# Performance work log

Hardware: AMD Instinct MI355X
Metric: run time of the kernel (lower is better)

## Reference

```python
import jax, jax.numpy as jnp
import numpy as np

ALPHA = 0.2  # LeakyReLU negative slope


def setup_inputs() -> dict:
    key = jax.random.key(0)
    ks = jax.random.split(key, 8)
    B, S, T, V, F = 8, 25, 64, 256, 256
    N = S * T
    h = jax.random.normal(ks[0], (B, S, T, V), dtype=jnp.float32)
    adj = jax.random.randint(ks[1], (N, N), 0, 2, dtype=jnp.int32)
    # xavier-ish scaling for stability
    W = jax.random.normal(ks[2], (F, V), dtype=jnp.float32) * (1.414 / np.sqrt(V))
    bW = jax.random.normal(ks[3], (F,), dtype=jnp.float32) * 0.01
    ai = jax.random.normal(ks[4], (1, F), dtype=jnp.float32) * (1.414 / np.sqrt(F))
    bi = jax.random.normal(ks[5], (1,), dtype=jnp.float32) * 0.01
    aj = jax.random.normal(ks[6], (1, F), dtype=jnp.float32) * (1.414 / np.sqrt(F))
    bj = jax.random.normal(ks[7], (1,), dtype=jnp.float32) * 0.01
    return {"h": h, "adj": adj, "W": W, "bW": bW, "ai": ai, "bi": bi, "aj": aj, "bj": bj}


def reference(h, adj, W, bW, ai, bi, aj, bj):
    B, S, T, V = h.shape
    N = S * T
    x = h.reshape(B, N, V)                    # [B, N, V]
    Wh = jnp.einsum('bnv,fv->bnf', x, W) + bW  # [B, N, F]
    Wh1 = jnp.einsum('bnf,of->bno', Wh, ai) + bi  # [B, N, 1]
    Wh2 = jnp.einsum('bnf,of->bno', Wh, aj) + bj  # [B, N, 1]
    e = Wh1 + jnp.swapaxes(Wh2, 1, 2)          # [B, N, N] additive scores
    e = jnp.where(e > 0, e, ALPHA * e)         # LeakyReLU
    att = jnp.where(adj[None, :, :] > 0, e, jnp.float32(-1e9))
    att = jax.nn.softmax(att, axis=2)          # masked softmax over neighbors
    h_hat = jnp.einsum('bij,bjf->bif', att, Wh)  # [B, N, F]
    return jax.nn.elu(h_hat)                   # concat=True path
```

## Files before the change

### kernel.cpp

```cpp
#include <hip/hip_runtime.h>
#include <hip/hip_bf16.h>

typedef __attribute__((ext_vector_type(8))) short bf16x8;
typedef __attribute__((ext_vector_type(4))) float f32x4;

#define LRELU_ALPHA 0.2f

static __device__ __forceinline__ unsigned short f2bf(float x) {
    unsigned u = __float_as_uint(x);
    u += 0x7fffu + ((u >> 16) & 1u);
    return (unsigned short)(u >> 16);
}
static __device__ __forceinline__ unsigned f2ord(float x) {
    unsigned b = __float_as_uint(x);
    return (b & 0x80000000u) ? ~b : (b | 0x80000000u);
}
static __device__ __forceinline__ float ord2f(unsigned m) {
    unsigned b = (m & 0x80000000u) ? (m ^ 0x80000000u) : ~m;
    return __uint_as_float(b);
}

__global__ __launch_bounds__(256) void k_convert(
    const float* __restrict__ x, const float* __restrict__ W,
    unsigned short* __restrict__ xb, unsigned short* __restrict__ Wb)
{
    const int bid = blockIdx.x;
    const float* src;
    unsigned short* dst;
    size_t base;
    if (bid < 1600) { src = x; dst = xb; base = (size_t)bid * 2048; }
    else            { src = W; dst = Wb; base = (size_t)(bid - 1600) * 2048; }
    const size_t idx = base + (size_t)threadIdx.x * 8;
    float4 v0 = *(const float4*)&src[idx];
    float4 v1 = *(const float4*)&src[idx + 4];
    ushort4 o0 = { f2bf(v0.x), f2bf(v0.y), f2bf(v0.z), f2bf(v0.w) };
    ushort4 o1 = { f2bf(v1.x), f2bf(v1.y), f2bf(v1.z), f2bf(v1.w) };
    *(ushort4*)&dst[idx]     = o0;
    *(ushort4*)&dst[idx + 4] = o1;
}

__global__ __launch_bounds__(256) void k_gemm_fused(
    const unsigned short* __restrict__ xb, const unsigned short* __restrict__ Wb,
    const float* __restrict__ bW, const float* __restrict__ ai,
    const float* __restrict__ bi, const float* __restrict__ aj,
    const float* __restrict__ bj,
    unsigned short* __restrict__ WhT, float* __restrict__ Wh1,
    float* __restrict__ Wh2, unsigned* __restrict__ M2g)
{
    __shared__ float part1[2][32], part2[2][32];
    const int t = threadIdx.x;
    const int w = t >> 6, l = t & 63;
    const int wr = w >> 1, wc = w & 1;
    const int R0 = blockIdx.x * 32;
    const int arow = R0 + wr*16 + (l & 15);
    const int kg8 = (l >> 4) * 8;

    f32x4 acc[8];
#pragma unroll
    for (int nf = 0; nf < 8; ++nf) acc[nf] = (f32x4){0.f,0.f,0.f,0.f};

#pragma unroll 2
    for (int k0 = 0; k0 < 256; k0 += 32) {
        bf16x8 af = *(const bf16x8*)&xb[(size_t)arow*256 + k0 + kg8];
#pragma unroll
        for (int nf = 0; nf < 8; ++nf) {
            bf16x8 bfv = *(const bf16x8*)&Wb[(size_t)(wc*128 + nf*16 + (l&15))*256 + k0 + kg8];
            acc[nf] = __builtin_amdgcn_mfma_f32_16x16x32_bf16(af, bfv, acc[nf], 0, 0, 0);
        }
    }

    const int b   = R0 / 1600;
    const int n0b = R0 - b*1600;
    const int rowg = wr*16 + (l>>4)*4;
    float p1[4] = {0,0,0,0}, p2[4] = {0,0,0,0};
#pragma unroll
    for (int nf = 0; nf < 8; ++nf) {
        const int f = wc*128 + nf*16 + (l & 15);
        const float bwv = bW[f], aiv = ai[f], ajv = aj[f];
        float vv[4];
#pragma unroll
        for (int e = 0; e < 4; ++e) {
            float v = acc[nf][e] + bwv;
            vv[e] = v;
            p1[e] = __builtin_fmaf(v, aiv, p1[e]);
            p2[e] = __builtin_fmaf(v, ajv, p2[e]);
        }
        ushort4 o4 = { f2bf(vv[0]), f2bf(vv[1]), f2bf(vv[2]), f2bf(vv[3]) };
        *(ushort4*)&WhT[((size_t)(b*256 + f))*1600 + n0b + rowg] = o4;
    }
#pragma unroll
    for (int m = 1; m < 16; m <<= 1)
#pragma unroll
        for (int e = 0; e < 4; ++e) {
            p1[e] += __shfl_xor(p1[e], m, 64);
            p2[e] += __shfl_xor(p2[e], m, 64);
        }
    if ((l & 15) == 0)
#pragma unroll
        for (int e = 0; e < 4; ++e) {
            part1[wc][rowg + e] = p1[e];
            part2[wc][rowg + e] = p2[e];
        }
    __syncthreads();
    if (t < 32) {
        float v1 = part1[0][t] + part1[1][t] + bi[0];
        float v2 = part2[0][t] + part2[1][t] + bj[0];
        Wh1[R0 + t] = v1;
        Wh2[R0 + t] = v2;
        unsigned o = f2ord(v2);
#pragma unroll
        for (int m = 1; m < 32; m <<= 1) {
            unsigned o2 = __shfl_xor(o, m, 64);
            o = (o2 > o) ? o2 : o;
        }
        if (t == 0) atomicMax(&M2g[b], o);
    }
}

__global__ __launch_bounds__(512) void k_attn(
    const unsigned short* __restrict__ WhT,
    const float* __restrict__ Wh1, const unsigned* __restrict__ M2g,
    const float* __restrict__ Wh2, const int* __restrict__ adj,
    float* __restrict__ out)
{
    __shared__ alignas(16) unsigned short pls[2][32*64];
    __shared__ float l_s[32];

    const int t = threadIdx.x;
    const int w = t >> 6, l = t & 63;
    const int b = blockIdx.x & 7;
    const int i0 = (blockIdx.x >> 3) * 32;

    const float m2v = ord2f(M2g[b]);
    float wh1r[4], mr[4];
#pragma unroll
    for (int r = 0; r < 4; ++r) {
        int gi = i0 + w*4 + r;
        wh1r[r] = Wh1[b*1600 + gi];
        float s = wh1r[r] + m2v;
        mr[r] = s > 0.f ? s : LRELU_ALPHA * s;
    }
    float lsum[4] = {0.f,0.f,0.f,0.f};
    f32x4 acc[2][2];
#pragma unroll
    for (int mi = 0; mi < 2; ++mi)
#pragma unroll
        for (int nf = 0; nf < 2; ++nf) acc[mi][nf] = (f32x4){0.f,0.f,0.f,0.f};

    const unsigned short* whtb = WhT + (size_t)b*256*1600;
    const unsigned short* bp0 = whtb + (size_t)(w*32 +  0 + (l&15))*1600 + (l>>4)*8;
    const unsigned short* bp1 = whtb + (size_t)(w*32 + 16 + (l&15))*1600 + (l>>4)*8;

    int ac[4]; float wcur; bf16x8 bc[2][2];
#pragma unroll
    for (int r = 0; r < 4; ++r) ac[r] = adj[(size_t)(i0 + w*4 + r)*1600 + l];
    wcur = Wh2[b*1600 + l];
    bc[0][0] = *(const bf16x8*)(bp0);      bc[0][1] = *(const bf16x8*)(bp0 + 32);
    bc[1][0] = *(const bf16x8*)(bp1);      bc[1][1] = *(const bf16x8*)(bp1 + 32);

    for (int jt = 0; jt < 25; ++jt) {
        const int cb = jt & 1;
        int an[4]; float wn; bf16x8 bn[2][2];
        if (jt < 24) {
            const int j1 = (jt + 1) * 64;
            bn[0][0] = *(const bf16x8*)(bp0 + j1);      bn[0][1] = *(const bf16x8*)(bp0 + j1 + 32);
            bn[1][0] = *(const bf16x8*)(bp1 + j1);      bn[1][1] = *(const bf16x8*)(bp1 + j1 + 32);
#pragma unroll
            for (int r = 0; r < 4; ++r)
                an[r] = adj[(size_t)(i0 + w*4 + r)*1600 + j1 + l];
            wn = Wh2[b*1600 + j1 + l];
        }
        __builtin_amdgcn_sched_barrier(0);
#pragma unroll
        for (int r = 0; r < 4; ++r) {
            const int row = w*4 + r;
            float s = wh1r[r] + wcur;
            s = s > 0.f ? s : LRELU_ALPHA * s;
            float p = (ac[r] > 0) ? __expf(s - mr[r]) : 0.f;
            lsum[r] += p;
            int off = (row*128 + l*2) ^ ((row & 7) << 4);
            *(unsigned short*)((char*)pls[cb] + off) = f2bf(p);
        }
        asm volatile("s_waitcnt lgkmcnt(0)" ::: "memory");
        __builtin_amdgcn_sched_barrier(0);
        __builtin_amdgcn_s_barrier();
#pragma unroll
        for (int kb = 0; kb < 2; ++kb) {
            bf16x8 af[2];
#pragma unroll
            for (int mi = 0; mi < 2; ++mi) {
                int ar = mi*16 + (l & 15);
                int aoff = (ar*128 + kb*64 + (l>>4)*16) ^ ((ar & 7) << 4);
                af[mi] = *(const bf16x8*)((const char*)pls[cb] + aoff);
            }
#pragma unroll
            for (int mi = 0; mi < 2; ++mi)
#pragma unroll
                for (int nf = 0; nf < 2; ++nf)
                    acc[mi][nf] = __builtin_amdgcn_mfma_f32_16x16x32_bf16(
                        af[mi], bc[nf][kb], acc[mi][nf], 0, 0, 0);
        }
        if (jt < 24) {
#pragma unroll
            for (int r = 0; r < 4; ++r) ac[r] = an[r];
            wcur = wn;
#pragma unroll
            for (int nf = 0; nf < 2; ++nf)
#pragma unroll
                for (int kb = 0; kb < 2; ++kb) bc[nf][kb] = bn[nf][kb];
        }
    }
#pragma unroll
    for (int s2 = 1; s2 < 64; s2 <<= 1)
#pragma unroll
        for (int r = 0; r < 4; ++r)
            lsum[r] += __shfl_xor(lsum[r], s2, 64);
    if (l == 0)
#pragma unroll
        for (int r = 0; r < 4; ++r) l_s[w*4 + r] = lsum[r];
    __syncthreads();
#pragma unroll
    for (int mi = 0; mi < 2; ++mi)
#pragma unroll
        for (int e = 0; e < 4; ++e) {
            const int row = mi*16 + (l>>4)*4 + e;
            const float rl = 1.f / l_s[row];
#pragma unroll
            for (int nf = 0; nf < 2; ++nf) {
                float v = acc[mi][nf][e] * rl;
                v = v > 0.f ? v : expm1f(v);
                out[(size_t)(b*1600 + i0 + row)*256 + w*32 + nf*16 + (l & 15)] = v;
            }
        }
}

extern "C" void kernel_launch(void* const* d_in, const int* in_sizes, int n_in,
                              void* d_out, int out_size, void* d_ws, size_t ws_size,
                              hipStream_t stream)
{
    const float* h  = (const float*)d_in[0];
    const int* adj  = (const int*)d_in[1];
    const float* W  = (const float*)d_in[2];
    const float* bW = (const float*)d_in[3];
    const float* ai = (const float*)d_in[4];
    const float* bi = (const float*)d_in[5];
    const float* aj = (const float*)d_in[6];
    const float* bj = (const float*)d_in[7];
    float* out = (float*)d_out;

    char* ws = (char*)d_ws;
    unsigned short* xb  = (unsigned short*)ws;
    unsigned short* Wb  = (unsigned short*)(ws + 6553600);
    unsigned short* WhT = (unsigned short*)(ws + 6684672);
    float* Wh1 = (float*)(ws + 13238272);
    float* Wh2 = (float*)(ws + 13289472);
    unsigned* M2g = (unsigned*)(ws + 13340672);

    hipMemsetAsync(M2g, 0, 32, stream);
    k_convert<<<1632, 256, 0, stream>>>(h, W, xb, Wb);
    k_gemm_fused<<<400, 256, 0, stream>>>(xb, Wb, bW, ai, bi, aj, bj,
                                          WhT, Wh1, Wh2, M2g);
    k_attn<<<400, 512, 0, stream>>>(WhT, Wh1, M2g, Wh2, adj, out);
}
```

Measured before the change: 162.2 us.

## Pack adjacency to bitmask, fuse x conversion into GEMM, restage attention with LDS-DMA pipeline

The separate fp32-to-bf16 conversion of h is removed and done inside the GEMM, and the GEMM now covers 64 rows by all 256 features per block. Adjacency is packed into a bitmask once per call, which shrinks the per-tile reads in the attention kernel. The attention kernel is rebuilt: 128 query rows by 128 features per block, WhT tiles staged into LDS with global_load_lds in a triple-buffered pipeline, probabilities built directly in registers as MFMA A operands, and exp2 with pre-scaled logits. It adds a prep kernel and relies on more complex synchronization, and rows are padded at the last tile (208 blocks).

```diff
diff --git a/kernel.cpp b/kernel.cpp
--- a/kernel.cpp
+++ b/kernel.cpp
@@ -4,7 +4,8 @@
 typedef __attribute__((ext_vector_type(8))) short bf16x8;
 typedef __attribute__((ext_vector_type(4))) float f32x4;
 
-#define LRELU_ALPHA 0.2f
+#define ALPHA 0.2f
+#define L2E 1.4426950408889634f
 
 static __device__ __forceinline__ unsigned short f2bf(float x) {
     unsigned u = __float_as_uint(x);
@@ -20,62 +21,77 @@
     return __uint_as_float(b);
 }
 
-__global__ __launch_bounds__(256) void k_convert(
-    const float* __restrict__ x, const float* __restrict__ W,
-    unsigned short* __restrict__ xb, unsigned short* __restrict__ Wb)
-{
-    const int bid = blockIdx.x;
-    const float* src;
-    unsigned short* dst;
-    size_t base;
-    if (bid < 1600) { src = x; dst = xb; base = (size_t)bid * 2048; }
-    else            { src = W; dst = Wb; base = (size_t)(bid - 1600) * 2048; }
-    const size_t idx = base + (size_t)threadIdx.x * 8;
-    float4 v0 = *(const float4*)&src[idx];
-    float4 v1 = *(const float4*)&src[idx + 4];
-    ushort4 o0 = { f2bf(v0.x), f2bf(v0.y), f2bf(v0.z), f2bf(v0.w) };
-    ushort4 o1 = { f2bf(v1.x), f2bf(v1.y), f2bf(v1.z), f2bf(v1.w) };
-    *(ushort4*)&dst[idx]     = o0;
-    *(ushort4*)&dst[idx + 4] = o1;
-}
-
-__global__ __launch_bounds__(256) void k_gemm_fused(
-    const unsigned short* __restrict__ xb, const unsigned short* __restrict__ Wb,
+__global__ __launch_bounds__(256) void k_prep(
+    const float* __restrict__ W, const int* __restrict__ adj,
+    unsigned short* __restrict__ Wb, unsigned* __restrict__ bm)
+{
+    const int bid = blockIdx.x, t = threadIdx.x;
+    if (bid < 32) {
+        const size_t idx = (size_t)bid * 2048 + (size_t)t * 8;
+        float4 v0 = *(const float4*)&W[idx];
+        float4 v1 = *(const float4*)&W[idx + 4];
+        ushort4 o0 = { f2bf(v0.x), f2bf(v0.y), f2bf(v0.z), f2bf(v0.w) };
+        ushort4 o1 = { f2bf(v1.x), f2bf(v1.y), f2bf(v1.z), f2bf(v1.w) };
+        *(ushort4*)&Wb[idx]     = o0;
+        *(ushort4*)&Wb[idx + 4] = o1;
+    } else {
+        const int w = t >> 6, l = t & 63;
+        const int row0 = (bid - 32) * 8 + w * 2;
+#pragma unroll
+        for (int rr = 0; rr < 2; ++rr) {
+            const int row = row0 + rr;
+            for (int ps = 0; ps < 25; ++ps) {
+                int a = adj[(size_t)row * 1600 + ps * 64 + l];
+                unsigned long long mask = __ballot(a > 0);
+                if (l == 0) {
+                    bm[row * 50 + ps * 2]     = (unsigned)mask;
+                    bm[row * 50 + ps * 2 + 1] = (unsigned)(mask >> 32);
+                }
+            }
+        }
+    }
+}
+
+__global__ __launch_bounds__(256) void k_gemm(
+    const float* __restrict__ x, const unsigned short* __restrict__ Wb,
     const float* __restrict__ bW, const float* __restrict__ ai,
     const float* __restrict__ bi, const float* __restrict__ aj,
     const float* __restrict__ bj,
-    unsigned short* __restrict__ WhT, float* __restrict__ Wh1,
-    float* __restrict__ Wh2, unsigned* __restrict__ M2g)
-{
-    __shared__ float part1[2][32], part2[2][32];
-    const int t = threadIdx.x;
-    const int w = t >> 6, l = t & 63;
-    const int wr = w >> 1, wc = w & 1;
-    const int R0 = blockIdx.x * 32;
-    const int arow = R0 + wr*16 + (l & 15);
-    const int kg8 = (l >> 4) * 8;
-
-    f32x4 acc[8];
-#pragma unroll
-    for (int nf = 0; nf < 8; ++nf) acc[nf] = (f32x4){0.f,0.f,0.f,0.f};
-
-#pragma unroll 2
+    unsigned short* __restrict__ WhT, float* __restrict__ W1L,
+    float* __restrict__ W2L, unsigned* __restrict__ M2g)
+{
+    const int t = threadIdx.x, w = t >> 6, l = t & 63;
+    const int R0 = blockIdx.x * 64;
+    const int rA = R0 + w * 16 + (l & 15);
+    const int kg = (l >> 4) * 8;
+
+    f32x4 acc[16];
+#pragma unroll
+    for (int nf = 0; nf < 16; ++nf) acc[nf] = (f32x4){0.f, 0.f, 0.f, 0.f};
+
+#pragma unroll
     for (int k0 = 0; k0 < 256; k0 += 32) {
-        bf16x8 af = *(const bf16x8*)&xb[(size_t)arow*256 + k0 + kg8];
-#pragma unroll
-        for (int nf = 0; nf < 8; ++nf) {
-            bf16x8 bfv = *(const bf16x8*)&Wb[(size_t)(wc*128 + nf*16 + (l&15))*256 + k0 + kg8];
-            acc[nf] = __builtin_amdgcn_mfma_f32_16x16x32_bf16(af, bfv, acc[nf], 0, 0, 0);
-        }
-    }
-
-    const int b   = R0 / 1600;
-    const int n0b = R0 - b*1600;
-    const int rowg = wr*16 + (l>>4)*4;
-    float p1[4] = {0,0,0,0}, p2[4] = {0,0,0,0};
-#pragma unroll
-    for (int nf = 0; nf < 8; ++nf) {
-        const int f = wc*128 + nf*16 + (l & 15);
+        float4 a0 = *(const float4*)&x[(size_t)rA * 256 + k0 + kg];
+        float4 a1 = *(const float4*)&x[(size_t)rA * 256 + k0 + kg + 4];
+        union { bf16x8 v; __hip_bfloat162 h[4]; } ua;
+        ua.h[0] = __float22bfloat162_rn(make_float2(a0.x, a0.y));
+        ua.h[1] = __float22bfloat162_rn(make_float2(a0.z, a0.w));
+        ua.h[2] = __float22bfloat162_rn(make_float2(a1.x, a1.y));
+        ua.h[3] = __float22bfloat162_rn(make_float2(a1.z, a1.w));
+        bf16x8 af = ua.v;
+#pragma unroll
+        for (int nf = 0; nf < 16; ++nf) {
+            bf16x8 bv = *(const bf16x8*)&Wb[(size_t)(nf * 16 + (l & 15)) * 256 + k0 + kg];
+            acc[nf] = __builtin_amdgcn_mfma_f32_16x16x32_bf16(af, bv, acc[nf], 0, 0, 0);
+        }
+    }
+
+    const int b = blockIdx.x / 25;
+    const int nloc = R0 - b * 1600 + w * 16 + (l >> 4) * 4;
+    float p1[4] = {0, 0, 0, 0}, p2[4] = {0, 0, 0, 0};
+#pragma unroll
+    for (int nf = 0; nf < 16; ++nf) {
+        const int f = nf * 16 + (l & 15);
         const float bwv = bW[f], aiv = ai[f], ajv = aj[f];
         float vv[4];
 #pragma unroll
@@ -86,7 +102,7 @@
             p2[e] = __builtin_fmaf(v, ajv, p2[e]);
         }
         ushort4 o4 = { f2bf(vv[0]), f2bf(vv[1]), f2bf(vv[2]), f2bf(vv[3]) };
-        *(ushort4*)&WhT[((size_t)(b*256 + f))*1600 + n0b + rowg] = o4;
+        *(ushort4*)&WhT[((size_t)(b * 256 + f)) * 1600 + nloc] = o4;
     }
 #pragma unroll
     for (int m = 1; m < 16; m <<= 1)
@@ -95,143 +111,172 @@
             p1[e] += __shfl_xor(p1[e], m, 64);
             p2[e] += __shfl_xor(p2[e], m, 64);
         }
-    if ((l & 15) == 0)
+    const float biv = bi[0], bjv = bj[0];
+    float v2s[4];
+#pragma unroll
+    for (int e = 0; e < 4; ++e) v2s[e] = (p2[e] + bjv) * L2E;
+    if ((l & 15) == 0) {
 #pragma unroll
         for (int e = 0; e < 4; ++e) {
-            part1[wc][rowg + e] = p1[e];
-            part2[wc][rowg + e] = p2[e];
-        }
-    __syncthreads();
-    if (t < 32) {
-        float v1 = part1[0][t] + part1[1][t] + bi[0];
-        float v2 = part2[0][t] + part2[1][t] + bj[0];
-        Wh1[R0 + t] = v1;
-        Wh2[R0 + t] = v2;
-        unsigned o = f2ord(v2);
-#pragma unroll
-        for (int m = 1; m < 32; m <<= 1) {
-            unsigned o2 = __shfl_xor(o, m, 64);
-            o = (o2 > o) ? o2 : o;
-        }
-        if (t == 0) atomicMax(&M2g[b], o);
-    }
+            int n = R0 + w * 16 + (l >> 4) * 4 + e;
+            W1L[n] = (p1[e] + biv) * L2E;
+            W2L[n] = v2s[e];
+        }
+    }
+    float m2 = fmaxf(fmaxf(v2s[0], v2s[1]), fmaxf(v2s[2], v2s[3]));
+    m2 = fmaxf(m2, __shfl_xor(m2, 16, 64));
+    m2 = fmaxf(m2, __shfl_xor(m2, 32, 64));
+    if (l == 0) atomicMax(&M2g[b], f2ord(m2));
+}
+
+struct Pref { float4 w2[2][2]; uint2 q; };
+
+static __device__ __forceinline__ void prefetchT(
+    Pref& P, int jt, const float* __restrict__ w2lp,
+    const unsigned char* __restrict__ bmrow, int l)
+{
+    const int g = (l >> 4) * 8;
+#pragma unroll
+    for (int kb = 0; kb < 2; ++kb) {
+        P.w2[kb][0] = *(const float4*)&w2lp[jt * 64 + kb * 32 + g];
+        P.w2[kb][1] = *(const float4*)&w2lp[jt * 64 + kb * 32 + g + 4];
+    }
+    P.q = *(const uint2*)&bmrow[jt * 8];
+}
+
+static __device__ __forceinline__ void stageT(
+    unsigned short* buf, int jt, const unsigned short* __restrict__ src,
+    int w, int l)
+{
+#pragma unroll
+    for (int q = 0; q < 2; ++q) {
+        const int f_loc = q * 64 + w * 8 + (l >> 3);
+        const int cs = (l & 7) ^ ((l >> 3) & 7);
+        const unsigned short* g = src + (size_t)f_loc * 1600 + jt * 64 + cs * 8;
+        __builtin_amdgcn_global_load_lds(
+            (const __attribute__((address_space(1))) unsigned int*)g,
+            (__attribute__((address_space(3))) unsigned int*)(buf + q * 4096 + w * 512),
+            16, 0, 0);
+    }
+    __builtin_amdgcn_sched_barrier(0);
+}
+
+static __device__ __forceinline__ void scoresT(
+    const Pref& P, float W1Lv, float mL, int l, bf16x8 af[2], float& lsum)
+{
+#pragma unroll
+    for (int kb = 0; kb < 2; ++kb) {
+        const unsigned byte = ((kb ? P.q.y : P.q.x) >> ((l >> 4) * 8)) & 0xffu;
+        float pf[8];
+#pragma unroll
+        for (int e = 0; e < 8; ++e) {
+            float w2 = ((const float*)&P.w2[kb][e >> 2])[e & 3];
+            float s = W1Lv + w2;
+            s = fmaxf(s, ALPHA * s);
+            float pm = exp2f(s - mL);
+            float p = ((byte >> e) & 1u) ? pm : 0.f;
+            lsum += p;
+            pf[e] = p;
+        }
+        union { bf16x8 v; __hip_bfloat162 h[4]; } u;
+#pragma unroll
+        for (int e2 = 0; e2 < 4; ++e2)
+            u.h[e2] = __float22bfloat162_rn(make_float2(pf[2 * e2], pf[2 * e2 + 1]));
+        af[kb] = u.v;
+    }
+}
+
+static __device__ __forceinline__ void pvT(
+    const unsigned short* buf, const bf16x8 af[2], f32x4* acc, int l)
+{
+    __builtin_amdgcn_sched_barrier(0);
+    __builtin_amdgcn_s_barrier();
+    __builtin_amdgcn_sched_barrier(0);
+#pragma unroll
+    for (int kb = 0; kb < 2; ++kb)
+#pragma unroll
+        for (int nf = 0; nf < 8; ++nf) {
+            const int f_loc = nf * 16 + (l & 15);
+            const int byte = f_loc * 128 + ((kb * 64 + (l >> 4) * 16) ^ ((f_loc & 7) << 4));
+            bf16x8 bv = *(const bf16x8*)((const char*)buf + byte);
+            acc[nf] = __builtin_amdgcn_mfma_f32_16x16x32_bf16(af[kb], bv, acc[nf], 0, 0, 0);
+        }
 }
 
 __global__ __launch_bounds__(512) void k_attn(
-    const unsigned short* __restrict__ WhT,
-    const float* __restrict__ Wh1, const unsigned* __restrict__ M2g,
-    const float* __restrict__ Wh2, const int* __restrict__ adj,
-    float* __restrict__ out)
-{
-    __shared__ alignas(16) unsigned short pls[2][32*64];
-    __shared__ float l_s[32];
-
-    const int t = threadIdx.x;
-    const int w = t >> 6, l = t & 63;
+    const unsigned short* __restrict__ WhT, const float* __restrict__ W1L,
+    const float* __restrict__ W2L, const unsigned* __restrict__ M2g,
+    const unsigned char* __restrict__ bmb, float* __restrict__ out)
+{
+    __shared__ alignas(16) unsigned short bufs[3][8192];
+
+    const int t = threadIdx.x, w = t >> 6, l = t & 63;
     const int b = blockIdx.x & 7;
-    const int i0 = (blockIdx.x >> 3) * 32;
-
-    const float m2v = ord2f(M2g[b]);
-    float wh1r[4], mr[4];
-#pragma unroll
-    for (int r = 0; r < 4; ++r) {
-        int gi = i0 + w*4 + r;
-        wh1r[r] = Wh1[b*1600 + gi];
-        float s = wh1r[r] + m2v;
-        mr[r] = s > 0.f ? s : LRELU_ALPHA * s;
-    }
-    float lsum[4] = {0.f,0.f,0.f,0.f};
-    f32x4 acc[2][2];
-#pragma unroll
-    for (int mi = 0; mi < 2; ++mi)
-#pragma unroll
-        for (int nf = 0; nf < 2; ++nf) acc[mi][nf] = (f32x4){0.f,0.f,0.f,0.f};
-
-    const unsigned short* whtb = WhT + (size_t)b*256*1600;
-    const unsigned short* bp0 = whtb + (size_t)(w*32 +  0 + (l&15))*1600 + (l>>4)*8;
-    const unsigned short* bp1 = whtb + (size_t)(w*32 + 16 + (l&15))*1600 + (l>>4)*8;
-
-    int ac[4]; float wcur; bf16x8 bc[2][2];
-#pragma unroll
-    for (int r = 0; r < 4; ++r) ac[r] = adj[(size_t)(i0 + w*4 + r)*1600 + l];
-    wcur = Wh2[b*1600 + l];
-    bc[0][0] = *(const bf16x8*)(bp0);      bc[0][1] = *(const bf16x8*)(bp0 + 32);
-    bc[1][0] = *(const bf16x8*)(bp1);      bc[1][1] = *(const bf16x8*)(bp1 + 32);
-
-    for (int jt = 0; jt < 25; ++jt) {
-        const int cb = jt & 1;
-        int an[4]; float wn; bf16x8 bn[2][2];
-        if (jt < 24) {
-            const int j1 = (jt + 1) * 64;
-            bn[0][0] = *(const bf16x8*)(bp0 + j1);      bn[0][1] = *(const bf16x8*)(bp0 + j1 + 32);
-            bn[1][0] = *(const bf16x8*)(bp1 + j1);      bn[1][1] = *(const bf16x8*)(bp1 + j1 + 32);
-#pragma unroll
-            for (int r = 0; r < 4; ++r)
-                an[r] = adj[(size_t)(i0 + w*4 + r)*1600 + j1 + l];
-            wn = Wh2[b*1600 + j1 + l];
-        }
-        __builtin_amdgcn_sched_barrier(0);
-#pragma unroll
-        for (int r = 0; r < 4; ++r) {
-            const int row = w*4 + r;
-            float s = wh1r[r] + wcur;
-            s = s > 0.f ? s : LRELU_ALPHA * s;
-            float p = (ac[r] > 0) ? __expf(s - mr[r]) : 0.f;
-            lsum[r] += p;
-            int off = (row*128 + l*2) ^ ((row & 7) << 4);
-            *(unsigned short*)((char*)pls[cb] + off) = f2bf(p);
-        }
-        asm volatile("s_waitcnt lgkmcnt(0)" ::: "memory");
-        __builtin_amdgcn_sched_barrier(0);
-        __builtin_amdgcn_s_barrier();
-#pragma unroll
-        for (int kb = 0; kb < 2; ++kb) {
-            bf16x8 af[2];
-#pragma unroll
-            for (int mi = 0; mi < 2; ++mi) {
-                int ar = mi*16 + (l & 15);
-                int aoff = (ar*128 + kb*64 + (l>>4)*16) ^ ((ar & 7) << 4);
-                af[mi] = *(const bf16x8*)((const char*)pls[cb] + aoff);
+    const int r = blockIdx.x >> 3;
+    const int it = r >> 1, fs = r & 1;
+    const int i0 = it * 128;
+
+    const int i_loc = i0 + w * 16 + (l & 15);
+    const int i_eff = i_loc < 1600 ? i_loc : 1599;
+    const float W1Lv = W1L[b * 1600 + i_eff];
+    const float M2Lv = ord2f(M2g[b]);
+    float mlt = W1Lv + M2Lv;
+    const float mL = fmaxf(mlt, ALPHA * mlt);
+
+    const unsigned short* src = WhT + (size_t)(b * 256 + fs * 128) * 1600;
+    const float* w2lp = W2L + b * 1600;
+    const unsigned char* bmrow = bmb + (size_t)i_eff * 200;
+
+    f32x4 acc[8];
+#pragma unroll
+    for (int nf = 0; nf < 8; ++nf) acc[nf] = (f32x4){0.f, 0.f, 0.f, 0.f};
+    float lsum = 0.f;
+    bf16x8 af[2];
+    Pref PA, PB, PC;
+
+    stageT(bufs[0], 0, src, w, l);
+    prefetchT(PA, 0, w2lp, bmrow, l);
+
+    int jt = 0;
+#pragma unroll 1
+    for (int u = 0; u < 8; ++u) {
+        stageT(bufs[1], jt + 1, src, w, l);
+        prefetchT(PB, jt + 1, w2lp, bmrow, l);
+        scoresT(PA, W1Lv, mL, l, af, lsum);
+        pvT(bufs[0], af, acc, l);
+
+        stageT(bufs[2], jt + 2, src, w, l);
+        prefetchT(PC, jt + 2, w2lp, bmrow, l);
+        scoresT(PB, W1Lv, mL, l, af, lsum);
+        pvT(bufs[1], af, acc, l);
+
+        stageT(bufs[0], jt + 3, src, w, l);
+        prefetchT(PA, jt + 3, w2lp, bmrow, l);
+        scoresT(PC, W1Lv, mL, l, af, lsum);
+        pvT(bufs[2], af, acc, l);
+        jt += 3;
+    }
+    scoresT(PA, W1Lv, mL, l, af, lsum);
+    pvT(bufs[0], af, acc, l);
+
+    lsum += __shfl_xor(lsum, 16, 64);
+    lsum += __shfl_xor(lsum, 32, 64);
+
+    if (i0 + w * 16 < 1600) {
+        float* op = out + ((size_t)b * 1600 + i0 + w * 16) * 256 + fs * 128;
+#pragma unroll
+        for (int e = 0; e < 4; ++e) {
+            const int rowl = (l >> 4) * 4 + e;
+            const float L = __shfl(lsum, rowl, 64);
+            const float rl = 1.f / L;
+#pragma unroll
+            for (int nf = 0; nf < 8; ++nf) {
+                float v = acc[nf][e] * rl;
+                v = v > 0.f ? v : expm1f(v);
+                op[(size_t)rowl * 256 + nf * 16 + (l & 15)] = v;
             }
-#pragma unroll
-            for (int mi = 0; mi < 2; ++mi)
-#pragma unroll
-                for (int nf = 0; nf < 2; ++nf)
-                    acc[mi][nf] = __builtin_amdgcn_mfma_f32_16x16x32_bf16(
-                        af[mi], bc[nf][kb], acc[mi][nf], 0, 0, 0);
-        }
-        if (jt < 24) {
-#pragma unroll
-            for (int r = 0; r < 4; ++r) ac[r] = an[r];
-            wcur = wn;
-#pragma unroll
-            for (int nf = 0; nf < 2; ++nf)
-#pragma unroll
-                for (int kb = 0; kb < 2; ++kb) bc[nf][kb] = bn[nf][kb];
-        }
-    }
-#pragma unroll
-    for (int s2 = 1; s2 < 64; s2 <<= 1)
-#pragma unroll
-        for (int r = 0; r < 4; ++r)
-            lsum[r] += __shfl_xor(lsum[r], s2, 64);
-    if (l == 0)
-#pragma unroll
-        for (int r = 0; r < 4; ++r) l_s[w*4 + r] = lsum[r];
-    __syncthreads();
-#pragma unroll
-    for (int mi = 0; mi < 2; ++mi)
-#pragma unroll
-        for (int e = 0; e < 4; ++e) {
-            const int row = mi*16 + (l>>4)*4 + e;
-            const float rl = 1.f / l_s[row];
-#pragma unroll
-            for (int nf = 0; nf < 2; ++nf) {
-                float v = acc[mi][nf][e] * rl;
-                v = v > 0.f ? v : expm1f(v);
-                out[(size_t)(b*1600 + i0 + row)*256 + w*32 + nf*16 + (l & 15)] = v;
-            }
-        }
+        }
+    }
 }
 
 extern "C" void kernel_launch(void* const* d_in, const int* in_sizes, int n_in,
@@ -249,16 +294,15 @@
     float* out = (float*)d_out;
 
     char* ws = (char*)d_ws;
-    unsigned short* xb  = (unsigned short*)ws;
-    unsigned short* Wb  = (unsigned short*)(ws + 6553600);
-    unsigned short* WhT = (unsigned short*)(ws + 6684672);
-    float* Wh1 = (float*)(ws + 13238272);
-    float* Wh2 = (float*)(ws + 13289472);
-    unsigned* M2g = (unsigned*)(ws + 13340672);
+    unsigned short* Wb  = (unsigned short*)ws;
+    unsigned*       bm  = (unsigned*)(ws + 131072);
+    unsigned short* WhT = (unsigned short*)(ws + 451072);
+    float* W1L = (float*)(ws + 7004672);
+    float* W2L = (float*)(ws + 7055872);
+    unsigned* M2g = (unsigned*)(ws + 7107072);
 
     hipMemsetAsync(M2g, 0, 32, stream);
-    k_convert<<<1632, 256, 0, stream>>>(h, W, xb, Wb);
-    k_gemm_fused<<<400, 256, 0, stream>>>(xb, Wb, bW, ai, bi, aj, bj,
-                                          WhT, Wh1, Wh2, M2g);
-    k_attn<<<400, 512, 0, stream>>>(WhT, Wh1, M2g, Wh2, adj, out);
-}
+    k_prep<<<232, 256, 0, stream>>>(W, adj, Wb, bm);
+    k_gemm<<<200, 256, 0, stream>>>(h, Wb, bW, ai, bi, aj, bj, WhT, W1L, W2L, M2g);
+    k_attn<<<208, 512, 0, stream>>>(WhT, W1L, W2L, M2g, (const unsigned char*)bm, out);
+}
```

Measured after the change: 171.4 us. 1.06x slower.
